# Performance work log

Hardware: AMD Instinct MI355X
Metric: run time of the kernel (lower is better)

The kernel has to match this reference:

```python
import jax, jax.numpy as jnp
import numpy as np

N_HEAD, D_HEAD, D_MODEL = 16, 64, 1024
BSZ, QLEN, MEMLEN = 4, 1024, 1024
KLEN = QLEN + MEMLEN
LN_EPS = 1e-5


def _rel_shift(x):
    # x: [b, q, k, n] -> Transformer-XL relative shift
    b, q, k, n = x.shape
    x = jnp.pad(x, ((0, 0), (0, 0), (1, 0), (0, 0)))  # [b, q, k+1, n]
    x = x.reshape(b, k + 1, q, n)[:, 1:]
    return x.reshape(b, q, k, n)


def _layer_norm(x, gamma, beta):
    mu = jnp.mean(x, axis=-1, keepdims=True)
    var = jnp.var(x, axis=-1, keepdims=True)
    return (x - mu) * jax.lax.rsqrt(var + LN_EPS) * gamma + beta


def setup_inputs() -> dict:
    key = jax.random.key(0)
    ks = jax.random.split(key, 8)
    w = jax.random.normal(ks[0], (BSZ, QLEN, D_MODEL), dtype=jnp.float32)
    r = jax.random.normal(ks[1], (1, KLEN, D_MODEL), dtype=jnp.float32)
    mem = jax.random.normal(ks[2], (BSZ, MEMLEN, D_MODEL), dtype=jnp.float32)
    # causal mask: key j visible iff j <= i + MEMLEN; 1 = masked
    i = jnp.arange(QLEN)[:, None]
    j = jnp.arange(KLEN)[None, :]
    attention_mask = (j > i + MEMLEN).astype(jnp.int32)
    s = 0.02
    qkv_w = jax.random.normal(ks[3], (3 * N_HEAD * D_HEAD, D_MODEL), dtype=jnp.float32) * s
    r_w = jax.random.normal(ks[4], (N_HEAD * D_HEAD, D_MODEL), dtype=jnp.float32) * s
    o_w = jax.random.normal(ks[5], (D_MODEL, N_HEAD * D_HEAD), dtype=jnp.float32) * s
    r_r_bias = jax.random.normal(ks[6], (N_HEAD, D_HEAD), dtype=jnp.float32) * s
    r_w_bias = jax.random.normal(ks[7], (N_HEAD, D_HEAD), dtype=jnp.float32) * s
    ln_gamma = jnp.ones((D_MODEL,), dtype=jnp.float32)
    ln_beta = jnp.zeros((D_MODEL,), dtype=jnp.float32)
    return {"w": w, "r": r, "mem": mem, "attention_mask": attention_mask,
            "qkv_w": qkv_w, "r_w": r_w, "o_w": o_w,
            "r_r_bias": r_r_bias, "r_w_bias": r_w_bias,
            "ln_gamma": ln_gamma, "ln_beta": ln_beta}


def reference(w, r, mem, attention_mask, qkv_w, r_w, o_w, r_r_bias, r_w_bias, ln_gamma, ln_beta):
    bsz, qlen, d_model = w.shape
    n_head, d_head = r_r_bias.shape
    scale = 1.0 / (d_head ** 0.5)
    cat = jnp.concatenate([mem, w], axis=1)                 # [b, klen, dm]
    heads = cat @ qkv_w.T                                   # post-lnorm: no pre-LN
    q, k, v = jnp.split(heads, 3, axis=-1)
    q = q[:, -qlen:]
    klen = k.shape[1]
    q = q.reshape(bsz, qlen, n_head, d_head)
    k = k.reshape(bsz, klen, n_head, d_head)
    v = v.reshape(bsz, klen, n_head, d_head)
    rk = (r @ r_w.T).reshape(-1, n_head, d_head)            # [rlen, n, d]
    AC = jnp.einsum('bind,bjnd->bijn', q + r_w_bias, k)
    BD = _rel_shift(jnp.einsum('bind,jnd->bijn', q + r_r_bias, rk))
    score = (AC + BD) * scale                               # [b, q, k, n]
    mask = (attention_mask == 1)[None, :, :, None]
    score = jnp.where(mask, -1e30, score)
    prob = jax.nn.softmax(score, axis=2)                    # softmax over keys
    vec = jnp.einsum('bijn,bjnd->bind', prob, v).reshape(bsz, qlen, n_head * d_head)
    attn_out = vec @ o_w.T
    # post layer-norm, deepnorm_alpha defaults to 1.0, dropout is identity (eval)
    return _layer_norm(w + attn_out, ln_gamma, ln_beta)
```

## Files before the change

### kernel.cpp

```cpp
#include <hip/hip_runtime.h>

typedef __attribute__((ext_vector_type(8))) __bf16 bf16x8;
typedef __attribute__((ext_vector_type(4))) __bf16 bf16x4;
typedef __attribute__((ext_vector_type(4))) float f32x4;
typedef __attribute__((ext_vector_type(16))) float f32x16;

#define SCALE_LOG2E 0.18033688011112042f

__device__ __forceinline__ f32x4 mfma16(bf16x8 a, bf16x8 b, f32x4 c) {
  return __builtin_amdgcn_mfma_f32_16x16x32_bf16(a, b, c, 0, 0, 0);
}
__device__ __forceinline__ f32x16 mfma32(bf16x8 a, bf16x8 b, f32x16 c) {
  return __builtin_amdgcn_mfma_f32_32x32x16_bf16(a, b, c, 0, 0, 0);
}

__device__ __forceinline__ void gload_lds16(const void* g, void* l) {
  __builtin_amdgcn_global_load_lds(
      (__attribute__((address_space(1))) void*)(void*)g,
      (__attribute__((address_space(3))) void*)l, 16, 0, 0);
}

__device__ __forceinline__ bf16x8 ldsfrag(const __bf16* base, int row, int lc) {
  return *(const bf16x8*)(base + row * 64 + ((lc ^ (row & 7)) << 3));
}


__global__ __launch_bounds__(256) void cast_plain(const float* __restrict__ in,
                                                  __bf16* __restrict__ out) {
  size_t t = (size_t)blockIdx.x * 256 + threadIdx.x;
  const float4* p = (const float4*)(in + t * 8);
  float4 a = p[0], b = p[1];
  bf16x8 v;
  v[0] = (__bf16)a.x; v[1] = (__bf16)a.y; v[2] = (__bf16)a.z; v[3] = (__bf16)a.w;
  v[4] = (__bf16)b.x; v[5] = (__bf16)b.y; v[6] = (__bf16)b.z; v[7] = (__bf16)b.w;
  *(bf16x8*)(out + t * 8) = v;
}

__global__ __launch_bounds__(256) void cast_cat(const float* __restrict__ mem,
                                                const float* __restrict__ w,
                                                __bf16* __restrict__ out) {
  size_t t = (size_t)blockIdx.x * 256 + threadIdx.x;
  size_t o = t * 8;
  int c = (int)(o & 1023);
  int row = (int)(o >> 10);
  int tt = row & 2047;
  int b = row >> 11;
  const float* src = (tt < 1024)
      ? (mem + ((size_t)(b * 1024 + tt) * 1024 + c))
      : (w + ((size_t)(b * 1024 + (tt - 1024)) * 1024 + c));
  float4 a = ((const float4*)src)[0], d = ((const float4*)src)[1];
  bf16x8 v;
  v[0] = (__bf16)a.x; v[1] = (__bf16)a.y; v[2] = (__bf16)a.z; v[3] = (__bf16)a.w;
  v[4] = (__bf16)d.x; v[5] = (__bf16)d.y; v[6] = (__bf16)d.z; v[7] = (__bf16)d.w;
  *(bf16x8*)(out + o) = v;
}

template <int MODE>
__global__ __launch_bounds__(256, 2) void gemm_bt(const __bf16* __restrict__ A,
                                                  const __bf16* __restrict__ B,
                                                  __bf16* __restrict__ Cb,
                                                  float* __restrict__ Cf,
                                                  const float* __restrict__ Res,
                                                  int M, int N, int K, int skipq) {
  if (skipq && blockIdx.x < 8 && (blockIdx.y & 15) < 8) return;
  __shared__ __bf16 As[128 * 32];
  __shared__ __bf16 Bs[128 * 32];
  const int tid = threadIdx.x;
  const int wid = tid >> 6, lane = tid & 63;
  const int l15 = lane & 15, lhi = lane >> 4;
  const int wr = wid >> 1, wc = wid & 1;
  const size_t arow0 = (size_t)blockIdx.y * 128;
  const size_t brow0 = (size_t)blockIdx.x * 128;

  f32x4 acc[4][4] = {};

  const int c0 = tid, c1 = tid + 256;
  const int r0 = c0 >> 2, o0 = (c0 & 3) * 8;
  const int r1 = c1 >> 2, o1 = (c1 & 3) * 8;
  const __bf16* ga0 = A + (arow0 + r0) * K + o0;
  const __bf16* ga1 = A + (arow0 + r1) * K + o1;
  const __bf16* gb0 = B + (brow0 + r0) * K + o0;
  const __bf16* gb1 = B + (brow0 + r1) * K + o1;
  __bf16* la0 = As + wid * 512;
  __bf16* la1 = As + 2048 + wid * 512;
  __bf16* lb0 = Bs + wid * 512;
  __bf16* lb1 = Bs + 2048 + wid * 512;

  for (int k0 = 0; k0 < K; k0 += 32) {
    gload_lds16(ga0 + k0, la0);
    gload_lds16(ga1 + k0, la1);
    gload_lds16(gb0 + k0, lb0);
    gload_lds16(gb1 + k0, lb1);
    __syncthreads();
    bf16x8 af[4], bf[4];
#pragma unroll
    for (int m = 0; m < 4; ++m)
      af[m] = *(const bf16x8*)(As + (wr * 64 + m * 16 + l15) * 32 + lhi * 8);
#pragma unroll
    for (int n = 0; n < 4; ++n)
      bf[n] = *(const bf16x8*)(Bs + (wc * 64 + n * 16 + l15) * 32 + lhi * 8);
#pragma unroll
    for (int m = 0; m < 4; ++m)
#pragma unroll
      for (int n = 0; n < 4; ++n)
        acc[m][n] = mfma16(af[m], bf[n], acc[m][n]);
    __syncthreads();
  }

#pragma unroll
  for (int m = 0; m < 4; ++m)
#pragma unroll
    for (int n = 0; n < 4; ++n) {
      size_t row = arow0 + wr * 64 + m * 16 + lhi * 4;
      size_t col = brow0 + wc * 64 + n * 16 + l15;
#pragma unroll
      for (int j = 0; j < 4; ++j) {
        size_t idx = (row + j) * (size_t)N + col;
        float v = acc[m][n][j];
        if (MODE == 0) Cb[idx] = (__bf16)v;
        else Cf[idx] = v + Res[idx];
      }
    }
}

__global__ __launch_bounds__(256) void vtrans_kernel(const __bf16* __restrict__ heads,
                                                     __bf16* __restrict__ vT) {
  __shared__ __bf16 T[64][66];
  const int j0 = blockIdx.x * 64;
  const int h = blockIdx.y, b = blockIdx.z;
  const int tid = threadIdx.x;
  {
    int jj = tid >> 2, dq = tid & 3;
    const __bf16* src = heads + ((size_t)(b * 2048 + j0 + jj)) * 3072 + 2048 + h * 64 + dq * 16;
    bf16x8 a = *(const bf16x8*)src;
    bf16x8 c = *(const bf16x8*)(src + 8);
#pragma unroll
    for (int e = 0; e < 8; ++e) { T[jj][dq * 16 + e] = a[e]; T[jj][dq * 16 + 8 + e] = c[e]; }
  }
  __syncthreads();
  {
    int d = tid >> 2, jq = tid & 3;
    bf16x8 o0, o1;
#pragma unroll
    for (int e = 0; e < 8; ++e) { o0[e] = T[jq * 16 + e][d]; o1[e] = T[jq * 16 + 8 + e][d]; }
    __bf16* dst = vT + ((size_t)((b * 16 + h) * 64 + d)) * 2048 + j0 + jq * 16;
    *(bf16x8*)dst = o0;
    *(bf16x8*)(dst + 8) = o1;
  }
}

__global__ __launch_bounds__(256) void ackb_kernel(const __bf16* __restrict__ heads,
                                                   const float* __restrict__ r_w_bias,
                                                   float* __restrict__ ackb) {
  int gid = blockIdx.x * 256 + threadIdx.x;
  int j = gid & 2047, bh = gid >> 11, b = bh >> 4, h = bh & 15;
  const __bf16* kp = heads + ((size_t)(b * 2048 + j)) * 3072 + 1024 + h * 64;
  const float* bw = r_w_bias + h * 64;
  float s = 0.f;
#pragma unroll
  for (int o = 0; o < 8; ++o) {
    bf16x8 kv = *(const bf16x8*)(kp + o * 8);
#pragma unroll
    for (int e = 0; e < 8; ++e) s += (float)kv[e] * bw[o * 8 + e];
  }
  ackb[(size_t)bh * 2048 + j] = s * SCALE_LOG2E;
}

__global__ __launch_bounds__(256) void brk_kernel(const __bf16* __restrict__ rk,
                                                  const float* __restrict__ r_r_bias,
                                                  float* __restrict__ brk) {
  int gid = blockIdx.x * 256 + threadIdx.x;
  int t = gid % 2304, h = gid / 2304;
  float s = 0.f;
  if (t < 2048) {
    const __bf16* rp = rk + (size_t)t * 1024 + h * 64;
    const float* br = r_r_bias + h * 64;
#pragma unroll
    for (int o = 0; o < 8; ++o) {
      bf16x8 rv = *(const bf16x8*)(rp + o * 8);
#pragma unroll
      for (int e = 0; e < 8; ++e) s += (float)rv[e] * br[o * 8 + e];
    }
  }
  brk[(size_t)h * 2304 + t] = s * SCALE_LOG2E;
}

__global__ __launch_bounds__(256, 2) void attn_kernel(
    const __bf16* __restrict__ heads, const __bf16* __restrict__ rk,
    const __bf16* __restrict__ vT, const float* __restrict__ ackb,
    const float* __restrict__ brk, __bf16* __restrict__ vec) {
  __shared__ __bf16 Ks[64 * 64];
  __shared__ __bf16 Rst[192 * 64];
  __shared__ __bf16 BP[4][3200];

  const int lin = blockIdx.x;
  const int xcd = lin & 7, s = lin >> 3;
  const int half = s >> 5, r5 = s & 31;
  const int bh = xcd * 8 + (r5 >> 3) + half * 4;
  const int bqr = r5 & 7;
  const int bq = half ? bqr : 7 - bqr;
  const int b = bh >> 4, h = bh & 15;
  const int base = bq << 7;

  const int tid = threadIdx.x;
  const int wid = tid >> 6, lane = tid & 63;
  const int il = lane & 31, hi5 = lane >> 5;
  const int i0 = base + wid * 32;

  const int srow8 = lane >> 3;
  const int sch = (lane & 7) ^ (srow8 & 7);

  bf16x8 qf[4];
  {
    const __bf16* qp =
        heads + ((size_t)(b * 2048 + 1024 + i0 + il)) * 3072 + h * 64 + hi5 * 8;
#pragma unroll
    for (int ks = 0; ks < 4; ++ks) {
      bf16x8 a = *(const bf16x8*)(qp + ks * 16);
      bf16x8 o;
#pragma unroll
      for (int e = 0; e < 8; ++e) o[e] = (__bf16)((float)a[e] * SCALE_LOG2E);
      qf[ks] = o;
    }
  }

  const float* ackbp = ackb + (size_t)bh * 2048;
  const float* brkp = brk + (size_t)h * 2304;
  const __bf16* vTp = vT + (size_t)bh * 64 * 2048;
  __bf16* Bw = BP[wid];

  float m_run = -1e30f, l_run = 0.f;
  f32x16 accv[2] = {};

  const int rkoff = 96 - wid * 32;
  const int jmaxb = min(2048, base + 1152);
  for (int j0 = 0; j0 < jmaxb; j0 += 64) {
    __syncthreads();
    {
      const __bf16* kst = heads +
          ((size_t)(b * 2048 + j0 + wid * 16 + srow8)) * 3072 + 1024 + h * 64 + sch * 8;
      gload_lds16(kst, Ks + (wid * 16) * 64);
      gload_lds16(kst + (size_t)8 * 3072, Ks + (wid * 16 + 8) * 64);
      const int rstart = j0 + 896 - base;
#pragma unroll
      for (int g = 0; g < 6; ++g) {
        int dr = wid * 48 + g * 8;
        int rg = min(rstart + dr + srow8, 2047);
        gload_lds16(rk + ((size_t)rg << 10) + h * 64 + sch * 8, Rst + dr * 64);
      }
    }
    __syncthreads();
    if (j0 >= i0 + 1056) continue;

    const int tbase = j0 + 992 - i0;

    bf16x8 vfr[4][2];
#pragma unroll
    for (int jc = 0; jc < 4; ++jc)
#pragma unroll
      for (int dt = 0; dt < 2; ++dt)
        vfr[jc][dt] = *(const bf16x8*)(vTp + (size_t)(dt * 32 + il) * 2048 +
                                       j0 + jc * 16 + hi5 * 8);

    __builtin_amdgcn_s_setprio(1);
#pragma unroll
    for (int ct = 0; ct < 3; ++ct) {
      f32x16 ci;
#pragma unroll
      for (int qd = 0; qd < 4; ++qd) {
        f32x4 b4 = *(const f32x4*)(brkp + tbase + ct * 32 + qd * 8 + hi5 * 4);
#pragma unroll
        for (int e = 0; e < 4; ++e) ci[qd * 4 + e] = b4[e];
      }
      const int ar = rkoff + ct * 32 + il;
#pragma unroll
      for (int ks = 0; ks < 4; ++ks)
        ci = mfma32(ldsfrag(Rst, ar, ks * 2 + hi5), qf[ks], ci);
#pragma unroll
      for (int qd = 0; qd < 4; ++qd) {
        union { unsigned u[2]; bf16x4 v; } pw;
        asm("v_cvt_pk_bf16_f32 %0, %1, %2"
            : "=v"(pw.u[0]) : "v"(ci[qd * 4 + 0]), "v"(ci[qd * 4 + 1]));
        asm("v_cvt_pk_bf16_f32 %0, %1, %2"
            : "=v"(pw.u[1]) : "v"(ci[qd * 4 + 2]), "v"(ci[qd * 4 + 3]));
        *(bf16x4*)(Bw + il * 100 + ct * 32 + qd * 8 + hi5 * 4) = pw.v;
      }
    }

    f32x16 st[2];
#pragma unroll
    for (int jt = 0; jt < 2; ++jt) {
      f32x16 ci;
#pragma unroll
      for (int qd = 0; qd < 4; ++qd) {
        f32x4 a4 = *(const f32x4*)(ackbp + j0 + jt * 32 + qd * 8 + hi5 * 4);
#pragma unroll
        for (int e = 0; e < 4; ++e) ci[qd * 4 + e] = a4[e];
      }
#pragma unroll
      for (int ks = 0; ks < 4; ++ks)
        ci = mfma32(ldsfrag(Ks, jt * 32 + il, ks * 2 + hi5), qf[ks], ci);
      st[jt] = ci;
    }
    __builtin_amdgcn_s_setprio(0);

    float sv[2][16];
#pragma unroll
    for (int jt = 0; jt < 2; ++jt)
#pragma unroll
      for (int rg = 0; rg < 16; ++rg) {
        const int crow = (rg & 3) + 8 * (rg >> 2) + 4 * hi5;
        const int c = jt * 32 + crow + 31 - il;
        sv[jt][rg] = st[jt][rg] + (float)Bw[il * 100 + c];
      }
    if (j0 + 63 > i0 + 1024) {
#pragma unroll
      for (int jt = 0; jt < 2; ++jt)
#pragma unroll
        for (int rg = 0; rg < 16; ++rg) {
          const int crow = (rg & 3) + 8 * (rg >> 2) + 4 * hi5;
          if (j0 + jt * 32 + crow > i0 + il + 1024) sv[jt][rg] = -1e30f;
        }
    }

    float mx = sv[0][0];
#pragma unroll
    for (int jt = 0; jt < 2; ++jt)
#pragma unroll
      for (int rg = 0; rg < 16; ++rg) mx = fmaxf(mx, sv[jt][rg]);
    mx = fmaxf(mx, __shfl_xor(mx, 32, 64));
    const bool resc = __any(mx > m_run + 8.0f);
    const float mn = resc ? fmaxf(m_run, mx) : m_run;
    float rs = 0.f;
#pragma unroll
    for (int jt = 0; jt < 2; ++jt)
#pragma unroll
      for (int rg = 0; rg < 16; ++rg) {
        float p = exp2f(sv[jt][rg] - mn);
        sv[jt][rg] = p;
        rs += p;
      }
    rs += __shfl_xor(rs, 32, 64);
    if (resc) {
      const float corr = exp2f(m_run - mn);
      m_run = mn;
      l_run = l_run * corr + rs;
      float c16[16];
#pragma unroll
      for (int rg = 0; rg < 16; ++rg) {
        const int crow = (rg & 3) + 8 * (rg >> 2) + 4 * hi5;
        c16[rg] = __shfl(corr, crow, 64);
      }
#pragma unroll
      for (int dt = 0; dt < 2; ++dt)
#pragma unroll
        for (int rg = 0; rg < 16; ++rg) accv[dt][rg] *= c16[rg];
    } else {
      l_run += rs;
    }

#pragma unroll
    for (int jt = 0; jt < 2; ++jt)
#pragma unroll
      for (int qd = 0; qd < 4; ++qd) {
        union { unsigned u[2]; bf16x4 v; } pw;
        asm("v_cvt_pk_bf16_f32 %0, %1, %2"
            : "=v"(pw.u[0]) : "v"(sv[jt][qd * 4 + 0]), "v"(sv[jt][qd * 4 + 1]));
        asm("v_cvt_pk_bf16_f32 %0, %1, %2"
            : "=v"(pw.u[1]) : "v"(sv[jt][qd * 4 + 2]), "v"(sv[jt][qd * 4 + 3]));
        *(bf16x4*)(Bw + il * 88 + jt * 32 + qd * 8 + hi5 * 4) = pw.v;
      }

    __builtin_amdgcn_s_setprio(1);
#pragma unroll
    for (int jc = 0; jc < 4; ++jc) {
      bf16x8 ap = *(const bf16x8*)(Bw + il * 88 + jc * 16 + hi5 * 8);
#pragma unroll
      for (int dt = 0; dt < 2; ++dt)
        accv[dt] = mfma32(ap, vfr[jc][dt], accv[dt]);
    }
    __builtin_amdgcn_s_setprio(0);
  }

  float linv[16];
#pragma unroll
  for (int rg = 0; rg < 16; ++rg) {
    const int crow = (rg & 3) + 8 * (rg >> 2) + 4 * hi5;
    linv[rg] = 1.0f / __shfl(l_run, crow, 64);
  }
#pragma unroll
  for (int dt = 0; dt < 2; ++dt)
#pragma unroll
    for (int rg = 0; rg < 16; ++rg) {
      const int crow = (rg & 3) + 8 * (rg >> 2) + 4 * hi5;
      vec[((size_t)(b * 1024 + i0 + crow)) * 1024 + h * 64 + dt * 32 + il] =
          (__bf16)(accv[dt][rg] * linv[rg]);
    }
}

__global__ __launch_bounds__(256) void ln_kernel(const float* __restrict__ pre,
                                                 const float* __restrict__ gamma,
                                                 const float* __restrict__ beta,
                                                 float* __restrict__ out) {
  const int row = blockIdx.x;
  const int tid = threadIdx.x;
  const float4 v = ((const float4*)(pre + (size_t)row * 1024))[tid];
  float s = v.x + v.y + v.z + v.w;
  float s2 = v.x * v.x + v.y * v.y + v.z * v.z + v.w * v.w;
#pragma unroll
  for (int off = 1; off < 64; off <<= 1) {
    s += __shfl_xor(s, off, 64);
    s2 += __shfl_xor(s2, off, 64);
  }
  __shared__ float red[8];
  const int wid = tid >> 6;
  if ((tid & 63) == 0) { red[wid * 2] = s; red[wid * 2 + 1] = s2; }
  __syncthreads();
  s = red[0] + red[2] + red[4] + red[6];
  s2 = red[1] + red[3] + red[5] + red[7];
  float mu = s * (1.0f / 1024.0f);
  float var = s2 * (1.0f / 1024.0f) - mu * mu;
  float rstd = rsqrtf(var + 1e-5f);
  float4 g = ((const float4*)gamma)[tid];
  float4 be = ((const float4*)beta)[tid];
  float4 o;
  o.x = (v.x - mu) * rstd * g.x + be.x;
  o.y = (v.y - mu) * rstd * g.y + be.y;
  o.z = (v.z - mu) * rstd * g.z + be.z;
  o.w = (v.w - mu) * rstd * g.w + be.w;
  ((float4*)(out + (size_t)row * 1024))[tid] = o;
}

extern "C" void kernel_launch(void* const* d_in, const int* in_sizes, int n_in,
                              void* d_out, int out_size, void* d_ws, size_t ws_size,
                              hipStream_t stream) {
  const float* w = (const float*)d_in[0];
  const float* r = (const float*)d_in[1];
  const float* mem = (const float*)d_in[2];
  const float* qkv_w = (const float*)d_in[4];
  const float* r_w = (const float*)d_in[5];
  const float* o_w = (const float*)d_in[6];
  const float* r_r_bias = (const float*)d_in[7];
  const float* r_w_bias = (const float*)d_in[8];
  const float* gamma = (const float*)d_in[9];
  const float* beta = (const float*)d_in[10];
  float* out = (float*)d_out;

  char* ws = (char*)d_ws;
  const size_t MB = 1024 * 1024;
  __bf16* catB = (__bf16*)(ws + 0);
  __bf16* vT = (__bf16*)(ws + 0);
  float* pre = (float*)(ws + 0);
  __bf16* qkvwB = (__bf16*)(ws + 16 * MB);
  __bf16* rB = (__bf16*)(ws + 22 * MB);
  __bf16* rwB = (__bf16*)(ws + 26 * MB);
  __bf16* owB = (__bf16*)(ws + 28 * MB);
  __bf16* headsB = (__bf16*)(ws + 30 * MB);
  __bf16* rkB = (__bf16*)(ws + 78 * MB);
  __bf16* vecB = (__bf16*)(ws + 82 * MB);
  float* ackbF = (float*)(ws + 90 * MB);
  float* brkF = (float*)(ws + 91 * MB);

  cast_cat<<<4096, 256, 0, stream>>>(mem, w, catB);
  cast_plain<<<1536, 256, 0, stream>>>(qkv_w, qkvwB);
  cast_plain<<<1024, 256, 0, stream>>>(r, rB);
  cast_plain<<<512, 256, 0, stream>>>(r_w, rwB);
  cast_plain<<<512, 256, 0, stream>>>(o_w, owB);

  gemm_bt<0><<<dim3(24, 64), 256, 0, stream>>>(catB, qkvwB, headsB, nullptr, nullptr,
                                               8192, 3072, 1024, 1);
  gemm_bt<0><<<dim3(8, 16), 256, 0, stream>>>(rB, rwB, rkB, nullptr, nullptr,
                                              2048, 1024, 1024, 0);

  vtrans_kernel<<<dim3(32, 16, 4), 256, 0, stream>>>(headsB, vT);
  ackb_kernel<<<512, 256, 0, stream>>>(headsB, r_w_bias, ackbF);
  brk_kernel<<<144, 256, 0, stream>>>(rkB, r_r_bias, brkF);

  attn_kernel<<<512, 256, 0, stream>>>(headsB, rkB, vT, ackbF, brkF, vecB);

  gemm_bt<1><<<dim3(8, 32), 256, 0, stream>>>(vecB, owB, nullptr, pre, w,
                                              4096, 1024, 1024, 0);
  ln_kernel<<<4096, 256, 0, stream>>>(pre, gamma, beta, out);
}
```

Before: 316.4 us.

## Double-buffer K tiles and use a ring buffer for rel-pos keys in attention

The attention loop now prefetches the next K tile into a second LDS buffer while the current tile is computed, cutting the two barriers per iteration to one. The relative-position key tile, which previously reloaded 192 rows every step, is kept in a 256-row LDS ring buffer, so each iteration fetches only the 64 new rows. This reduces redundant global-to-LDS traffic and exposed load latency. The cost is more shared memory per block (higher LDS footprint could affect occupancy at 2 blocks/CU) and more reliance on the async LDS loads completing before the single barrier.

Measured after the change: 324.6 us. 2.6% more time.

```diff
diff --git a/kernel.cpp b/kernel.cpp
--- a/kernel.cpp
+++ b/kernel.cpp
@@ -189,8 +189,8 @@
     const __bf16* __restrict__ heads, const __bf16* __restrict__ rk,
     const __bf16* __restrict__ vT, const float* __restrict__ ackb,
     const float* __restrict__ brk, __bf16* __restrict__ vec) {
-  __shared__ __bf16 Ks[64 * 64];
-  __shared__ __bf16 Rst[192 * 64];
+  __shared__ __bf16 Ks[2 * 4096];
+  __shared__ __bf16 Ring[256 * 64];
   __shared__ __bf16 BP[4][3200];
 
   const int lin = blockIdx.x;
@@ -229,157 +229,176 @@
   const __bf16* vTp = vT + (size_t)bh * 64 * 2048;
   __bf16* Bw = BP[wid];
 
+  {
+    const __bf16* kst = heads +
+        ((size_t)(b * 2048 + wid * 16 + srow8)) * 3072 + 1024 + h * 64 + sch * 8;
+    gload_lds16(kst, Ks + (wid * 16) * 64);
+    gload_lds16(kst + (size_t)8 * 3072, Ks + (wid * 16 + 8) * 64);
+    const int rbase = 896 - base;
+#pragma unroll
+    for (int g = 0; g < 6; ++g) {
+      const int r = rbase + wid * 48 + g * 8;
+      const int rg = min(r + srow8, 2047);
+      gload_lds16(rk + ((size_t)rg << 10) + h * 64 + sch * 8,
+                  Ring + (size_t)(r & 255) * 64);
+    }
+  }
+  __syncthreads();
+
   float m_run = -1e30f, l_run = 0.f;
   f32x16 accv[2] = {};
 
-  const int rkoff = 96 - wid * 32;
   const int jmaxb = min(2048, base + 1152);
   for (int j0 = 0; j0 < jmaxb; j0 += 64) {
-    __syncthreads();
-    {
+    const int sbuf = (j0 >> 6) & 1;
+
+    if (j0 + 64 < jmaxb) {
+      const int jn = j0 + 64;
       const __bf16* kst = heads +
-          ((size_t)(b * 2048 + j0 + wid * 16 + srow8)) * 3072 + 1024 + h * 64 + sch * 8;
-      gload_lds16(kst, Ks + (wid * 16) * 64);
-      gload_lds16(kst + (size_t)8 * 3072, Ks + (wid * 16 + 8) * 64);
-      const int rstart = j0 + 896 - base;
-#pragma unroll
-      for (int g = 0; g < 6; ++g) {
-        int dr = wid * 48 + g * 8;
-        int rg = min(rstart + dr + srow8, 2047);
-        gload_lds16(rk + ((size_t)rg << 10) + h * 64 + sch * 8, Rst + dr * 64);
+          ((size_t)(b * 2048 + jn + wid * 16 + srow8)) * 3072 + 1024 + h * 64 + sch * 8;
+      gload_lds16(kst, Ks + (sbuf ^ 1) * 4096 + (wid * 16) * 64);
+      gload_lds16(kst + (size_t)8 * 3072, Ks + (sbuf ^ 1) * 4096 + (wid * 16 + 8) * 64);
+      const int T0 = j0 + 1088 - base;
+      const int r0 = T0 + wid * 16;
+      gload_lds16(rk + ((size_t)min(r0 + srow8, 2047) << 10) + h * 64 + sch * 8,
+                  Ring + (size_t)(r0 & 255) * 64);
+      gload_lds16(rk + ((size_t)min(r0 + 8 + srow8, 2047) << 10) + h * 64 + sch * 8,
+                  Ring + (size_t)((r0 + 8) & 255) * 64);
+    }
+
+    if (j0 < i0 + 1056) {
+      const __bf16* KsC = Ks + sbuf * 4096;
+      const int tbase = j0 + 992 - i0;
+
+      bf16x8 vfr[4][2];
+#pragma unroll
+      for (int jc = 0; jc < 4; ++jc)
+#pragma unroll
+        for (int dt = 0; dt < 2; ++dt)
+          vfr[jc][dt] = *(const bf16x8*)(vTp + (size_t)(dt * 32 + il) * 2048 +
+                                         j0 + jc * 16 + hi5 * 8);
+
+      __builtin_amdgcn_s_setprio(1);
+#pragma unroll
+      for (int ct = 0; ct < 3; ++ct) {
+        f32x16 ci;
+#pragma unroll
+        for (int qd = 0; qd < 4; ++qd) {
+          f32x4 b4 = *(const f32x4*)(brkp + tbase + ct * 32 + qd * 8 + hi5 * 4);
+#pragma unroll
+          for (int e = 0; e < 4; ++e) ci[qd * 4 + e] = b4[e];
+        }
+        const int slot = (tbase + ct * 32 + il) & 255;
+#pragma unroll
+        for (int ks = 0; ks < 4; ++ks)
+          ci = mfma32(ldsfrag(Ring, slot, ks * 2 + hi5), qf[ks], ci);
+#pragma unroll
+        for (int qd = 0; qd < 4; ++qd) {
+          union { unsigned u[2]; bf16x4 v; } pw;
+          asm("v_cvt_pk_bf16_f32 %0, %1, %2"
+              : "=v"(pw.u[0]) : "v"(ci[qd * 4 + 0]), "v"(ci[qd * 4 + 1]));
+          asm("v_cvt_pk_bf16_f32 %0, %1, %2"
+              : "=v"(pw.u[1]) : "v"(ci[qd * 4 + 2]), "v"(ci[qd * 4 + 3]));
+          *(bf16x4*)(Bw + il * 100 + ct * 32 + qd * 8 + hi5 * 4) = pw.v;
+        }
       }
-    }
-    __syncthreads();
-    if (j0 >= i0 + 1056) continue;
-
-    const int tbase = j0 + 992 - i0;
-
-    bf16x8 vfr[4][2];
-#pragma unroll
-    for (int jc = 0; jc < 4; ++jc)
-#pragma unroll
-      for (int dt = 0; dt < 2; ++dt)
-        vfr[jc][dt] = *(const bf16x8*)(vTp + (size_t)(dt * 32 + il) * 2048 +
-                                       j0 + jc * 16 + hi5 * 8);
-
-    __builtin_amdgcn_s_setprio(1);
-#pragma unroll
-    for (int ct = 0; ct < 3; ++ct) {
-      f32x16 ci;
-#pragma unroll
-      for (int qd = 0; qd < 4; ++qd) {
-        f32x4 b4 = *(const f32x4*)(brkp + tbase + ct * 32 + qd * 8 + hi5 * 4);
-#pragma unroll
-        for (int e = 0; e < 4; ++e) ci[qd * 4 + e] = b4[e];
+
+      f32x16 st[2];
+#pragma unroll
+      for (int jt = 0; jt < 2; ++jt) {
+        f32x16 ci;
+#pragma unroll
+        for (int qd = 0; qd < 4; ++qd) {
+          f32x4 a4 = *(const f32x4*)(ackbp + j0 + jt * 32 + qd * 8 + hi5 * 4);
+#pragma unroll
+          for (int e = 0; e < 4; ++e) ci[qd * 4 + e] = a4[e];
+        }
+#pragma unroll
+        for (int ks = 0; ks < 4; ++ks)
+          ci = mfma32(ldsfrag(KsC, jt * 32 + il, ks * 2 + hi5), qf[ks], ci);
+        st[jt] = ci;
       }
-      const int ar = rkoff + ct * 32 + il;
-#pragma unroll
-      for (int ks = 0; ks < 4; ++ks)
-        ci = mfma32(ldsfrag(Rst, ar, ks * 2 + hi5), qf[ks], ci);
-#pragma unroll
-      for (int qd = 0; qd < 4; ++qd) {
-        union { unsigned u[2]; bf16x4 v; } pw;
-        asm("v_cvt_pk_bf16_f32 %0, %1, %2"
-            : "=v"(pw.u[0]) : "v"(ci[qd * 4 + 0]), "v"(ci[qd * 4 + 1]));
-        asm("v_cvt_pk_bf16_f32 %0, %1, %2"
-            : "=v"(pw.u[1]) : "v"(ci[qd * 4 + 2]), "v"(ci[qd * 4 + 3]));
-        *(bf16x4*)(Bw + il * 100 + ct * 32 + qd * 8 + hi5 * 4) = pw.v;
-      }
-    }
-
-    f32x16 st[2];
-#pragma unroll
-    for (int jt = 0; jt < 2; ++jt) {
-      f32x16 ci;
-#pragma unroll
-      for (int qd = 0; qd < 4; ++qd) {
-        f32x4 a4 = *(const f32x4*)(ackbp + j0 + jt * 32 + qd * 8 + hi5 * 4);
-#pragma unroll
-        for (int e = 0; e < 4; ++e) ci[qd * 4 + e] = a4[e];
-      }
-#pragma unroll
-      for (int ks = 0; ks < 4; ++ks)
-        ci = mfma32(ldsfrag(Ks, jt * 32 + il, ks * 2 + hi5), qf[ks], ci);
-      st[jt] = ci;
-    }
-    __builtin_amdgcn_s_setprio(0);
-
-    float sv[2][16];
-#pragma unroll
-    for (int jt = 0; jt < 2; ++jt)
-#pragma unroll
-      for (int rg = 0; rg < 16; ++rg) {
-        const int crow = (rg & 3) + 8 * (rg >> 2) + 4 * hi5;
-        const int c = jt * 32 + crow + 31 - il;
-        sv[jt][rg] = st[jt][rg] + (float)Bw[il * 100 + c];
-      }
-    if (j0 + 63 > i0 + 1024) {
+      __builtin_amdgcn_s_setprio(0);
+
+      float sv[2][16];
 #pragma unroll
       for (int jt = 0; jt < 2; ++jt)
 #pragma unroll
         for (int rg = 0; rg < 16; ++rg) {
           const int crow = (rg & 3) + 8 * (rg >> 2) + 4 * hi5;
-          if (j0 + jt * 32 + crow > i0 + il + 1024) sv[jt][rg] = -1e30f;
-        }
-    }
-
-    float mx = sv[0][0];
-#pragma unroll
-    for (int jt = 0; jt < 2; ++jt)
-#pragma unroll
-      for (int rg = 0; rg < 16; ++rg) mx = fmaxf(mx, sv[jt][rg]);
-    mx = fmaxf(mx, __shfl_xor(mx, 32, 64));
-    const bool resc = __any(mx > m_run + 8.0f);
-    const float mn = resc ? fmaxf(m_run, mx) : m_run;
-    float rs = 0.f;
-#pragma unroll
-    for (int jt = 0; jt < 2; ++jt)
-#pragma unroll
-      for (int rg = 0; rg < 16; ++rg) {
-        float p = exp2f(sv[jt][rg] - mn);
-        sv[jt][rg] = p;
-        rs += p;
+          const int c = jt * 32 + crow + 31 - il;
+          sv[jt][rg] = st[jt][rg] + (float)Bw[il * 100 + c];
+        }
+      if (j0 + 63 > i0 + 1024) {
+#pragma unroll
+        for (int jt = 0; jt < 2; ++jt)
+#pragma unroll
+          for (int rg = 0; rg < 16; ++rg) {
+            const int crow = (rg & 3) + 8 * (rg >> 2) + 4 * hi5;
+            if (j0 + jt * 32 + crow > i0 + il + 1024) sv[jt][rg] = -1e30f;
+          }
       }
-    rs += __shfl_xor(rs, 32, 64);
-    if (resc) {
-      const float corr = exp2f(m_run - mn);
-      m_run = mn;
-      l_run = l_run * corr + rs;
-      float c16[16];
-#pragma unroll
-      for (int rg = 0; rg < 16; ++rg) {
-        const int crow = (rg & 3) + 8 * (rg >> 2) + 4 * hi5;
-        c16[rg] = __shfl(corr, crow, 64);
+
+      float mx = sv[0][0];
+#pragma unroll
+      for (int jt = 0; jt < 2; ++jt)
+#pragma unroll
+        for (int rg = 0; rg < 16; ++rg) mx = fmaxf(mx, sv[jt][rg]);
+      mx = fmaxf(mx, __shfl_xor(mx, 32, 64));
+      const bool resc = __any(mx > m_run + 8.0f);
+      const float mn = resc ? fmaxf(m_run, mx) : m_run;
+      float rs = 0.f;
+#pragma unroll
+      for (int jt = 0; jt < 2; ++jt)
+#pragma unroll
+        for (int rg = 0; rg < 16; ++rg) {
+          float p = exp2f(sv[jt][rg] - mn);
+          sv[jt][rg] = p;
+          rs += p;
+        }
+      rs += __shfl_xor(rs, 32, 64);
+      if (resc) {
+        const float corr = exp2f(m_run - mn);
+        m_run = mn;
+        l_run = l_run * corr + rs;
+        float c16[16];
+#pragma unroll
+        for (int rg = 0; rg < 16; ++rg) {
+          const int crow = (rg & 3) + 8 * (rg >> 2) + 4 * hi5;
+          c16[rg] = __shfl(corr, crow, 64);
+        }
+#pragma unroll
+        for (int dt = 0; dt < 2; ++dt)
+#pragma unroll
+          for (int rg = 0; rg < 16; ++rg) accv[dt][rg] *= c16[rg];
+      } else {
+        l_run += rs;
       }
-#pragma unroll
-      for (int dt = 0; dt < 2; ++dt)
-#pragma unroll
-        for (int rg = 0; rg < 16; ++rg) accv[dt][rg] *= c16[rg];
-    } else {
-      l_run += rs;
-    }
-
-#pragma unroll
-    for (int jt = 0; jt < 2; ++jt)
-#pragma unroll
-      for (int qd = 0; qd < 4; ++qd) {
-        union { unsigned u[2]; bf16x4 v; } pw;
-        asm("v_cvt_pk_bf16_f32 %0, %1, %2"
-            : "=v"(pw.u[0]) : "v"(sv[jt][qd * 4 + 0]), "v"(sv[jt][qd * 4 + 1]));
-        asm("v_cvt_pk_bf16_f32 %0, %1, %2"
-            : "=v"(pw.u[1]) : "v"(sv[jt][qd * 4 + 2]), "v"(sv[jt][qd * 4 + 3]));
-        *(bf16x4*)(Bw + il * 88 + jt * 32 + qd * 8 + hi5 * 4) = pw.v;
+
+#pragma unroll
+      for (int jt = 0; jt < 2; ++jt)
+#pragma unroll
+        for (int qd = 0; qd < 4; ++qd) {
+          union { unsigned u[2]; bf16x4 v; } pw;
+          asm("v_cvt_pk_bf16_f32 %0, %1, %2"
+              : "=v"(pw.u[0]) : "v"(sv[jt][qd * 4 + 0]), "v"(sv[jt][qd * 4 + 1]));
+          asm("v_cvt_pk_bf16_f32 %0, %1, %2"
+              : "=v"(pw.u[1]) : "v"(sv[jt][qd * 4 + 2]), "v"(sv[jt][qd * 4 + 3]));
+          *(bf16x4*)(Bw + il * 88 + jt * 32 + qd * 8 + hi5 * 4) = pw.v;
+        }
+
+      __builtin_amdgcn_s_setprio(1);
+#pragma unroll
+      for (int jc = 0; jc < 4; ++jc) {
+        bf16x8 ap = *(const bf16x8*)(Bw + il * 88 + jc * 16 + hi5 * 8);
+#pragma unroll
+        for (int dt = 0; dt < 2; ++dt)
+          accv[dt] = mfma32(ap, vfr[jc][dt], accv[dt]);
       }
-
-    __builtin_amdgcn_s_setprio(1);
-#pragma unroll
-    for (int jc = 0; jc < 4; ++jc) {
-      bf16x8 ap = *(const bf16x8*)(Bw + il * 88 + jc * 16 + hi5 * 8);
-#pragma unroll
-      for (int dt = 0; dt < 2; ++dt)
-        accv[dt] = mfma32(ap, vfr[jc][dt], accv[dt]);
-    }
-    __builtin_amdgcn_s_setprio(0);
+      __builtin_amdgcn_s_setprio(0);
+    }
+
+    __syncthreads();
   }
 
   float linv[16];
```
